# Kernel optimization log

Hardware: AMD Instinct MI355X
Metric: run time of the kernel (lower is better)

Reference implementation:

```python
import jax, jax.numpy as jnp
import numpy as np

B, T, I = 256, 1024, 64
P, E, NOUT = 256, 128, 64
K = 2
TEMP = 8.0
LN_EPS = 1e-5


def setup_inputs() -> dict:
    key = jax.random.key(0)
    ks = jax.random.split(key, 10)
    lim_in = 1.0 / np.sqrt(I)
    lim_e = 1.0 / np.sqrt(E)
    return {
        "x": jax.random.normal(ks[0], (B, T, I), dtype=jnp.float32),
        "pointer_init": jax.random.uniform(ks[1], (B,), dtype=jnp.float32) * P,
        "W_in": jax.random.uniform(ks[2], (E, I), minval=-lim_in, maxval=lim_in),
        "b_in": jax.random.uniform(ks[3], (E,), minval=-lim_in, maxval=lim_in),
        "ln_w": jnp.ones((E,), jnp.float32),
        "ln_b": jnp.zeros((E,), jnp.float32),
        "jump_dest": jax.random.uniform(ks[4], (P,), dtype=jnp.float32) * P,
        "Wg": jax.random.uniform(ks[5], (1, E), minval=-lim_e, maxval=lim_e),
        "bg": jax.random.uniform(ks[6], (1,), minval=-lim_e, maxval=lim_e),
        "context_strength": jnp.float32(0.2),
        "Wo": jax.random.uniform(ks[7], (NOUT, E), minval=-lim_e, maxval=lim_e),
        "bo": jax.random.uniform(ks[8], (NOUT,), minval=-lim_e, maxval=lim_e),
    }


def _layer_norm(h, w, b):
    mu = jnp.mean(h, axis=-1, keepdims=True)
    var = jnp.mean((h - mu) ** 2, axis=-1, keepdims=True)
    return (h - mu) * jax.lax.rsqrt(var + LN_EPS) * w + b


def reference(x, pointer_init, W_in, b_in, ln_w, ln_b, jump_dest, Wg, bg, context_strength, Wo, bo):
    Bsz = x.shape[0]
    nP = jump_dest.shape[0]
    offsets = jnp.arange(-K, K + 1, dtype=jnp.int32)  # [5]
    batch_idx = jnp.arange(Bsz)[:, None]               # [B,1]
    ctx_scale = jax.nn.sigmoid(context_strength)
    half = nP / 2.0

    def step(carry, x_t):
        mem, hid, ptr = carry                          # [B,P,E], [B,E], [B]
        emb = jnp.tanh(x_t @ W_in.T + b_in)            # [B,E]
        base = jnp.clip(jnp.floor(ptr).astype(jnp.int32), 0, nP - 1)
        idx = jnp.mod(base[:, None] + offsets[None, :], nP)  # [B,5]
        delta = jnp.mod(idx.astype(x_t.dtype) - ptr[:, None] + half, nP) - half
        w = jax.nn.softmax(-(delta ** 2) / TEMP, axis=1)     # [B,5]
        nbh = jnp.take_along_axis(mem, idx[:, :, None], axis=1)  # [B,5,E]
        ctx = jnp.sum(w[:, :, None] * nbh, axis=1)               # [B,E]
        su = jnp.tanh(emb + ctx_scale * ctx + hid)               # [B,E]
        hid_new = _layer_norm(su, ln_w, ln_b)
        mem_new = mem.at[batch_idx, idx].add(w[:, :, None] * su[:, None, :])
        cur = jnp.clip(ptr.astype(jnp.int32), 0, nP - 1)
        jt = jump_dest[cur]                                      # [B]
        jl = (su @ Wg.T + bg)[:, 0]                              # [B]
        probs = jax.nn.sigmoid(jl)
        sj = (probs > 0.5).astype(x_t.dtype) - jax.lax.stop_gradient(probs) + probs
        walk = jnp.mod(ptr + 1.0, nP)
        ptr_new = jnp.where(sj > 0.5, jt, walk)
        return (mem_new, hid_new, ptr_new), None

    mem0 = jnp.zeros((Bsz, nP, W_in.shape[0]), x.dtype)
    hid0 = jnp.zeros((Bsz, W_in.shape[0]), x.dtype)
    (mem, hid, ptr), _ = jax.lax.scan(step, (mem0, hid0, pointer_init), jnp.swapaxes(x, 0, 1))
    logits = hid @ Wo.T + bo
    return logits
```

## Files before the change

kernel.cpp:

```cpp
#include <hip/hip_runtime.h>
#include <math.h>

#define Bn    256
#define Tn    1024
#define In    64
#define Pn    256
#define En    128
#define NOUTn 64
#define LN_EPS 1e-5f

#define C1f 0.3606737602222409f
#define K1f 0.8824969025845955f
#define K2f 0.6065306597126334f

typedef float f32x2 __attribute__((ext_vector_type(2)));

__device__ __forceinline__ float tanh_fast(float x) {
    float e = __builtin_amdgcn_exp2f(x * 2.88539008177793f);
    return 1.0f - 2.0f * __builtin_amdgcn_rcpf(e + 1.0f);
}
__device__ __forceinline__ f32x2 tanh2(f32x2 x) {
    f32x2 e;
    e[0] = __builtin_amdgcn_exp2f(x[0] * 2.88539008177793f);
    e[1] = __builtin_amdgcn_exp2f(x[1] * 2.88539008177793f);
    f32x2 r;
    r[0] = __builtin_amdgcn_rcpf(e[0] + 1.0f);
    r[1] = __builtin_amdgcn_rcpf(e[1] + 1.0f);
    return 1.0f - 2.0f * r;
}

template<int CTRL, int RMASK>
__device__ __forceinline__ float dpp_add(float x) {
    return x + __int_as_float(__builtin_amdgcn_update_dpp(
        0, __float_as_int(x), CTRL, RMASK, 0xF, false));
}
__device__ __forceinline__ void wave_sum64_x3(float& x, float& y, float& z) {
#define LVL(C, R) x = dpp_add<C, R>(x); y = dpp_add<C, R>(y); z = dpp_add<C, R>(z);
    LVL(0x111, 0xF)
    LVL(0x112, 0xF)
    LVL(0x114, 0xF)
    LVL(0x118, 0xF)
    LVL(0x142, 0xA)
    LVL(0x143, 0xC)
#undef LVL
    x = __int_as_float(__builtin_amdgcn_readlane(__float_as_int(x), 63));
    y = __int_as_float(__builtin_amdgcn_readlane(__float_as_int(y), 63));
    z = __int_as_float(__builtin_amdgcn_readlane(__float_as_int(z), 63));
}

#define LDSF_FLOATS (Pn * En + Pn)
#define LDSF_BYTES  (LDSF_FLOATS * 4)

__global__ __launch_bounds__(192, 1)
void fused_kernel(const float* __restrict__ x,
                  const float* __restrict__ pointer_init,
                  const float* __restrict__ W_in, const float* __restrict__ b_in,
                  const float* __restrict__ ln_w, const float* __restrict__ ln_b,
                  const float* __restrict__ jump_dest,
                  const float* __restrict__ Wg,  const float* __restrict__ bg,
                  const float* __restrict__ cs_ptr,
                  const float* __restrict__ Wo,  const float* __restrict__ bo,
                  float* __restrict__ emb4, float* __restrict__ out) {
    extern __shared__ float lds[];
    float* mem = lds;
    float* jd  = lds + Pn * En;

    const int b   = blockIdx.x;
    const int tid = threadIdx.x;

    if (tid >= 64) {
        const int p     = tid - 64;
        const int t_oct = p >> 4;
        const int e0    = p & 15;
        float be[8];
        #pragma unroll
        for (int j = 0; j < 8; ++j) be[j] = b_in[e0 + 16 * j];

        const float* xb   = x + (size_t)b * Tn * In;
        float*       dstb = emb4 + ((size_t)b << 17);

#define PRODUCE(K) {                                                          \
    const int t0 = (K) * 64 + t_oct * 8;                                      \
    const float4* xr = (const float4*)(xb + t0 * In);      \
    float acc[8][8];                                                          \
    _Pragma("unroll")                                                         \
    for (int tt = 0; tt < 8; ++tt)                                            \
        _Pragma("unroll")                                                     \
        for (int j = 0; j < 8; ++j) acc[tt][j] = 0.f;                         \
    for (int i4 = 0; i4 < 16; ++i4) {                                         \
        float4 xv[8];                                                         \
        _Pragma("unroll")                                                     \
        for (int tt = 0; tt < 8; ++tt) xv[tt] = xr[tt * 16 + i4];             \
        float4 wf[8];                                                         \
        _Pragma("unroll")                                                     \
        for (int j = 0; j < 8; ++j)                                           \
            wf[j] = *(const float4*)(W_in + (e0 + 16 * j) * In + i4 * 4);     \
        _Pragma("unroll")                                                     \
        for (int tt = 0; tt < 8; ++tt)                                        \
            _Pragma("unroll")                                                 \
            for (int j = 0; j < 8; ++j) {                                     \
                acc[tt][j] += xv[tt].x * wf[j].x;                             \
                acc[tt][j] += xv[tt].y * wf[j].y;                             \
                acc[tt][j] += xv[tt].z * wf[j].z;                             \
                acc[tt][j] += xv[tt].w * wf[j].w;                             \
            }                                                                 \
    }                                                                         \
    const int tb0 = t0 >> 2;                                                  \
    _Pragma("unroll")                                                         \
    for (int j = 0; j < 8; ++j) {                                             \
        const int e = e0 + 16 * j;                                            \
        _Pragma("unroll")                                                     \
        for (int tb = 0; tb < 2; ++tb) {                                      \
            float4 o;                                                         \
            o.x = tanh_fast(acc[tb * 4 + 0][j] + be[j]);                      \
            o.y = tanh_fast(acc[tb * 4 + 1][j] + be[j]);                      \
            o.z = tanh_fast(acc[tb * 4 + 2][j] + be[j]);                      \
            o.w = tanh_fast(acc[tb * 4 + 3][j] + be[j]);                      \
            *(float4*)&dstb[((size_t)(tb0 + tb) * 128 + e) * 4] = o;          \
        }                                                                     \
    }                                                                         \
}
        PRODUCE(0)
        PRODUCE(1)
        __syncthreads();
        for (int k = 0; k < 16; ++k) {
            if (k + 2 < 16) PRODUCE(k + 2)
            __syncthreads();
        }
#undef PRODUCE
        __syncthreads();
        return;
    }

    const int l = tid;

    float4* m4 = (float4*)mem;
    for (int i = l; i < Pn * En / 4; i += 64) m4[i] = make_float4(0.f, 0.f, 0.f, 0.f);
    for (int i = l; i < Pn; i += 64) jd[i] = jump_dest[i];

    const f32x2 lnw = {ln_w[l], ln_w[l + 64]};
    const f32x2 lnb = {ln_b[l], ln_b[l + 64]};
    const f32x2 wg  = {Wg[l],   Wg[l + 64]};
    const float bgs = bg[0];
    const float cs  = 1.0f / (1.0f + expf(-cs_ptr[0]));
    f32x2 hid = {0.f, 0.f};

    float* myb = mem + 2 * l;

    float jl      = 1.0f;
    float jt_cur  = pointer_init[b];
    float ptrW    = 0.f;
    int   baseW   = 0;
    float jtW_pre = 0.f;
    float z0 = 0.f, z1 = 0.f, z2 = 1.f, z3 = 0.f, z4 = 0.f, inv = 1.f;
    f32x2 wnb0 = {0,0}, wnb1 = {0,0}, wnb2 = {0,0}, wnb3 = {0,0}, wnb4 = {0,0};
    float *wp0 = myb, *wp1 = myb, *wp2 = myb, *wp3 = myb, *wp4 = myb;

    __syncthreads();

    const float4* e40 = (const float4*)(emb4 + ((size_t)b << 17)) + l;
    const float4* e41 = e40 + 64;
    float4 A0 = e40[0],   A1 = e41[0];
    float4 B0 = e40[128], B1 = e41[128];

#define SSTEP(EC0, EC1) {                                                      \
    float ptr; int base;                                                       \
    f32x2 nb0, nb1, nb2, nb3, nb4;                                             \
    float *p0, *p1, *p2, *p3, *p4;                                             \
    float jt_nxt;                                                              \
    if (__builtin_amdgcn_readfirstlane(__float_as_int(jl)) > 0) {              \
                                     \
        ptr  = jt_cur;                                                         \
        base = (int)ptr; base = base > 255 ? 255 : base;                       \
        p0 = mem + (((base + 254) & 255) << 7) + 2 * l;                        \
        p1 = mem + (((base + 255) & 255) << 7) + 2 * l;                        \
        p2 = mem + (base << 7) + 2 * l;                                        \
        p3 = mem + (((base + 1) & 255) << 7) + 2 * l;                          \
        p4 = mem + (((base + 2) & 255) << 7) + 2 * l;                          \
        nb0 = *(f32x2*)p0; nb1 = *(f32x2*)p1; nb2 = *(f32x2*)p2;               \
        nb3 = *(f32x2*)p3; nb4 = *(f32x2*)p4;                                  \
        jt_nxt = jd[base];                                                     \
        const float frac = ptr - (float)base;                                  \
        const float r  = __builtin_amdgcn_exp2f(frac * C1f);                   \
        const float ri = __builtin_amdgcn_exp2f(-frac * C1f);                  \
        z0 = K2f * ri * ri; z1 = K1f * ri; z2 = 1.0f;                          \
        z3 = K1f * r;       z4 = K2f * r * r;                                  \
        inv = __builtin_amdgcn_rcpf(((z0 + z1) + (z2 + z3)) + z4);             \
    } else {                                                                   \
          \
        ptr = ptrW; base = baseW;                                              \
        nb0 = wnb0; nb1 = wnb1; nb2 = wnb2; nb3 = wnb3; nb4 = wnb4;            \
        p0 = wp0; p1 = wp1; p2 = wp2; p3 = wp3; p4 = wp4;                      \
        jt_nxt = jtW_pre;                                                      \
    }                                                                          \
    const f32x2 ctx = inv * (((nb0 * z0 + nb1 * z1) + (nb2 * z2 + nb3 * z3))   \
                             + nb4 * z4);                                      \
    f32x2 em; em[0] = (EC0); em[1] = (EC1);                                    \
    const f32x2 su = tanh2(em + cs * ctx + hid);                               \
    const f32x2 g  = su * inv;                                                 \
    const f32x2 m0v = nb0 + z0 * g, m1v = nb1 + z1 * g, m2v = nb2 + z2 * g,    \
                m3v = nb3 + z3 * g, m4v = nb4 + z4 * g;                        \
    *(f32x2*)p0 = m0v; *(f32x2*)p1 = m1v; *(f32x2*)p2 = m2v;                   \
    *(f32x2*)p3 = m3v; *(f32x2*)p4 = m4v;                                      \
     \
    baseW = (base + 1) & 255;                                                  \
    ptrW  = ptr + 1.0f; if (ptrW >= 256.0f) ptrW -= 256.0f;                    \
    wnb0 = m1v; wnb1 = m2v; wnb2 = m3v; wnb3 = m4v;                            \
    wp0 = p1; wp1 = p2; wp2 = p3; wp3 = p4;                                    \
    wp4 = mem + (((base + 3) & 255) << 7) + 2 * l;                             \
    wnb4 = *(f32x2*)wp4;                                                       \
    jtW_pre = jd[baseW];                                                       \
    jt_cur  = jt_nxt;                                                          \
                                                   \
    float s1 = su[0] + su[1];                                                  \
    const f32x2 sq = su * su;  float s2 = sq[0] + sq[1];                       \
    const f32x2 sg = su * wg;  float s3 = sg[0] + sg[1];                       \
    wave_sum64_x3(s1, s2, s3);                                                 \
    const float mu   = s1 * (1.0f / En);                                       \
    const float var  = s2 * (1.0f / En) - mu * mu;                             \
    const float rstd = __builtin_amdgcn_rsqf(var + LN_EPS);                    \
    hid = (su - mu) * rstd * lnw + lnb;                                        \
    jl  = s3 + bgs;                                                            \
}

    for (int k = 0; k < 16; ++k) {
        for (int tbi = 0; tbi < 16; ++tbi) {
            const int tb = k * 16 + tbi;
            const int tp = tb + 2 > 255 ? 255 : tb + 2;
            float4 C0 = e40[tp << 7];
            float4 C1 = e41[tp << 7];
            SSTEP(A0.x, A1.x)
            SSTEP(A0.y, A1.y)
            SSTEP(A0.z, A1.z)
            SSTEP(A0.w, A1.w)
            A0 = B0; A1 = B1; B0 = C0; B1 = C1;
        }
        __syncthreads();
    }
#undef SSTEP

    mem[l] = hid[0]; mem[64 + l] = hid[1];
    __syncthreads();
    const float4* w4 = (const float4*)(Wo + l * En);
    const float4* h4 = (const float4*)mem;
    float a0 = 0.f, a1 = 0.f, a2 = 0.f, a3 = 0.f;
    #pragma unroll
    for (int i = 0; i < En / 4; ++i) {
        float4 wv = w4[i]; float4 hv = h4[i];
        a0 += wv.x * hv.x; a1 += wv.y * hv.y; a2 += wv.z * hv.z; a3 += wv.w * hv.w;
    }
    out[b * NOUTn + l] = (a0 + a1) + (a2 + a3) + bo[l];
}

#define LDS_FLOATS (Pn*En + 2*En + 2*In + Pn)
#define LDS_BYTES  (LDS_FLOATS * 4)

__global__ __launch_bounds__(192, 1)
void ring_kernel(const float* __restrict__ x,
                 const float* __restrict__ pointer_init,
                 const float* __restrict__ W_in,
                 const float* __restrict__ b_in,
                 const float* __restrict__ ln_w,
                 const float* __restrict__ ln_b,
                 const float* __restrict__ jump_dest,
                 const float* __restrict__ Wg,
                 const float* __restrict__ bg,
                 const float* __restrict__ cs_ptr,
                 const float* __restrict__ Wo,
                 const float* __restrict__ bo,
                 float* __restrict__ out)
{
    extern __shared__ float lds[];
    float* mem  = lds;
    float* embb = mem + Pn * En;
    float* xb   = embb + 2 * En;
    float* jd   = xb + 2 * In;

    const int b   = blockIdx.x;
    const int tid = threadIdx.x;

    for (int i = tid; i < Pn * En; i += 192) mem[i] = 0.0f;
    for (int i = tid; i < Pn;      i += 192) jd[i]  = jump_dest[i];

    const float* xrow = x + (size_t)b * Tn * In;
    if (tid < 64) {
        xb[tid]      = xrow[tid];
        xb[In + tid] = xrow[In + tid];
    }
    __syncthreads();

    if (tid >= 64) {
        const int p = tid - 64;
        float wr[In];
        {
            const float4* w4 = (const float4*)(W_in + p * In);
            #pragma unroll
            for (int i = 0; i < In / 4; ++i) {
                float4 v = w4[i];
                wr[4*i+0] = v.x; wr[4*i+1] = v.y; wr[4*i+2] = v.z; wr[4*i+3] = v.w;
            }
        }
        const float bi = b_in[p];
        {
            float acc = bi;
            #pragma unroll
            for (int i = 0; i < In; ++i) acc += wr[i] * xb[i];
            embb[p] = tanhf(acc);
        }
        __syncthreads();
        for (int t = 0; t < Tn; ++t) {
            if (t + 1 < Tn) {
                const float* xc = xb + ((t + 1) & 1) * In;
                float acc = bi;
                #pragma unroll
                for (int i = 0; i < In; ++i) acc += wr[i] * xc[i];
                embb[((t + 1) & 1) * En + p] = tanhf(acc);
            }
            __syncthreads();
        }
    } else {
        const int l = tid;
        const float lnw0 = ln_w[l],      lnw1 = ln_w[l + 64];
        const float lnb0 = ln_b[l],      lnb1 = ln_b[l + 64];
        const float wg0  = Wg[l],        wg1  = Wg[l + 64];
        const float bgs  = bg[0];
        const float cs   = 1.0f / (1.0f + expf(-cs_ptr[0]));
        float hid0 = 0.0f, hid1 = 0.0f;
        float ptr  = pointer_init[b];
        __syncthreads();

        for (int t = 0; t < Tn; ++t) {
            const bool do_stage = (t + 2 < Tn);
            float xs = 0.0f;
            if (do_stage) xs = xrow[(t + 2) * In + l];

            const float* embc = embb + (t & 1) * En;

            int base = (int)floorf(ptr);
            base = base < 0 ? 0 : (base > Pn - 1 ? Pn - 1 : base);
            int cur = (int)ptr;
            cur = cur < 0 ? 0 : (cur > Pn - 1 ? Pn - 1 : cur);
            const float jt = jd[cur];

            const float frac = ptr - (float)base;
            int   idx[5];
            float wgt[5];
            float mx = -3.4e38f;
            #pragma unroll
            for (int j = 0; j < 5; ++j) {
                idx[j] = (base + j - 2 + Pn) & (Pn - 1);
                float d = (float)(j - 2) - frac;
                float s = -(d * d) * 0.125f;
                wgt[j] = s;
                mx = fmaxf(mx, s);
            }
            float se = 0.0f;
            #pragma unroll
            for (int j = 0; j < 5; ++j) { float ez = expf(wgt[j] - mx); wgt[j] = ez; se += ez; }
            const float inv = 1.0f / se;

            float nb0[5], nb1[5];
            #pragma unroll
            for (int j = 0; j < 5; ++j) {
                nb0[j] = mem[idx[j] * En + l];
                nb1[j] = mem[idx[j] * En + 64 + l];
            }
            float ctx0 = 0.0f, ctx1 = 0.0f;
            #pragma unroll
            for (int j = 0; j < 5; ++j) {
                const float w = wgt[j] * inv; wgt[j] = w;
                ctx0 += w * nb0[j];
                ctx1 += w * nb1[j];
            }

            const float su0 = tanhf(embc[l]      + cs * ctx0 + hid0);
            const float su1 = tanhf(embc[l + 64] + cs * ctx1 + hid1);

            #pragma unroll
            for (int j = 0; j < 5; ++j) {
                mem[idx[j] * En + l]      = nb0[j] + wgt[j] * su0;
                mem[idx[j] * En + 64 + l] = nb1[j] + wgt[j] * su1;
            }

            float s1 = su0 + su1;
            float s2 = su0 * su0 + su1 * su1;
            float s3 = su0 * wg0 + su1 * wg1;
            #pragma unroll
            for (int off = 32; off > 0; off >>= 1) {
                s1 += __shfl_xor(s1, off, 64);
                s2 += __shfl_xor(s2, off, 64);
                s3 += __shfl_xor(s3, off, 64);
            }

            const float mu   = s1 * (1.0f / En);
            const float var  = s2 * (1.0f / En) - mu * mu;
            const float rstd = rsqrtf(var + LN_EPS);
            hid0 = (su0 - mu) * rstd * lnw0 + lnb0;
            hid1 = (su1 - mu) * rstd * lnw1 + lnb1;

            const float jl = s3 + bgs;
            float walk = ptr + 1.0f;
            if (walk >= 256.0f) walk -= 256.0f;
            ptr = (jl > 0.0f) ? jt : walk;

            if (do_stage) xb[(t & 1) * In + l] = xs;
            __syncthreads();
        }
        embb[l]      = hid0;
        embb[l + 64] = hid1;
    }
    __syncthreads();

    if (tid < NOUTn) {
        const float* wrow = Wo + tid * En;
        float acc = bo[tid];
        #pragma unroll 4
        for (int e = 0; e < En; ++e) acc += embb[e] * wrow[e];
        out[b * NOUTn + tid] = acc;
    }
}

extern "C" void kernel_launch(void* const* d_in, const int* in_sizes, int n_in,
                              void* d_out, int out_size, void* d_ws, size_t ws_size,
                              hipStream_t stream) {
    const float* x            = (const float*)d_in[0];
    const float* pointer_init = (const float*)d_in[1];
    const float* W_in         = (const float*)d_in[2];
    const float* b_in         = (const float*)d_in[3];
    const float* ln_w         = (const float*)d_in[4];
    const float* ln_b         = (const float*)d_in[5];
    const float* jump_dest    = (const float*)d_in[6];
    const float* Wg           = (const float*)d_in[7];
    const float* bg           = (const float*)d_in[8];
    const float* cs           = (const float*)d_in[9];
    const float* Wo           = (const float*)d_in[10];
    const float* bo           = (const float*)d_in[11];
    float* out = (float*)d_out;

    const size_t emb_bytes = (size_t)Bn * Tn * En * sizeof(float);

    if (ws_size >= emb_bytes) {
        float* emb4 = (float*)d_ws;
        (void)hipFuncSetAttribute((const void*)fused_kernel,
                                  hipFuncAttributeMaxDynamicSharedMemorySize, LDSF_BYTES);
        fused_kernel<<<Bn, 192, LDSF_BYTES, stream>>>(
            x, pointer_init, W_in, b_in, ln_w, ln_b, jump_dest, Wg, bg, cs,
            Wo, bo, emb4, out);
    } else {
        (void)hipFuncSetAttribute((const void*)ring_kernel,
                                  hipFuncAttributeMaxDynamicSharedMemorySize, LDS_BYTES);
        ring_kernel<<<Bn, 192, LDS_BYTES, stream>>>(
            x, pointer_init, W_in, b_in, ln_w, ln_b, jump_dest, Wg, bg, cs, Wo, bo, out);
    }
}
```

Measured before the change: 504.6 us.

## Stage input embeddings in an LDS ring buffer instead of global workspace

```diff
diff --git a/kernel.cpp b/kernel.cpp
--- a/kernel.cpp
+++ b/kernel.cpp
@@ -48,83 +48,84 @@
     z = __int_as_float(__builtin_amdgcn_readlane(__float_as_int(z), 63));
 }
 
-#define LDSF_FLOATS (Pn * En + Pn)
-#define LDSF_BYTES  (LDSF_FLOATS * 4)
+#define STAGE_FLOATS (3 * 16 * En)
+#define LDSF_FLOATS  (Pn * En + Pn + STAGE_FLOATS)
+#define LDSF_BYTES   (LDSF_FLOATS * 4)
 
 __global__ __launch_bounds__(192, 1)
-void fused_kernel(const float* __restrict__ x,
-                  const float* __restrict__ pointer_init,
-                  const float* __restrict__ W_in, const float* __restrict__ b_in,
-                  const float* __restrict__ ln_w, const float* __restrict__ ln_b,
-                  const float* __restrict__ jump_dest,
-                  const float* __restrict__ Wg,  const float* __restrict__ bg,
-                  const float* __restrict__ cs_ptr,
-                  const float* __restrict__ Wo,  const float* __restrict__ bo,
-                  float* __restrict__ emb4, float* __restrict__ out) {
+void fused2_kernel(const float* __restrict__ x,
+                   const float* __restrict__ pointer_init,
+                   const float* __restrict__ W_in, const float* __restrict__ b_in,
+                   const float* __restrict__ ln_w, const float* __restrict__ ln_b,
+                   const float* __restrict__ jump_dest,
+                   const float* __restrict__ Wg,  const float* __restrict__ bg,
+                   const float* __restrict__ cs_ptr,
+                   const float* __restrict__ Wo,  const float* __restrict__ bo,
+                   float* __restrict__ out) {
     extern __shared__ float lds[];
     float* mem = lds;
     float* jd  = lds + Pn * En;
+    float* stg = lds + Pn * En + Pn;
 
     const int b   = blockIdx.x;
     const int tid = threadIdx.x;
 
     if (tid >= 64) {
-        const int p     = tid - 64;
-        const int t_oct = p >> 4;
-        const int e0    = p & 15;
-        float be[8];
+        const int p    = tid - 64;
+        const int tq   = p >> 5;
+        const int eidx = p & 31;
+        float be[4];
         #pragma unroll
-        for (int j = 0; j < 8; ++j) be[j] = b_in[e0 + 16 * j];
-
-        const float* xb   = x + (size_t)b * Tn * In;
-        float*       dstb = emb4 + ((size_t)b << 17);
-
-#define PRODUCE(K) {                                                          \
-    const int t0 = (K) * 64 + t_oct * 8;                                      \
+        for (int j = 0; j < 4; ++j) be[j] = b_in[eidx + 32 * j];
+        const float* xb = x + (size_t)b * Tn * In;
+
+#define PRODUCE(K, BUF) {                                                     \
+    const int t0 = (K) * 16 + tq * 4;                                         \
     const float4* xr = (const float4*)(xb + t0 * In);      \
-    float acc[8][8];                                                          \
+    float acc[4][4];                                                          \
     _Pragma("unroll")                                                         \
-    for (int tt = 0; tt < 8; ++tt)                                            \
-        _Pragma("unroll")                                                     \
-        for (int j = 0; j < 8; ++j) acc[tt][j] = 0.f;                         \
+    for (int tt = 0; tt < 4; ++tt)                                            \
+        _Pragma("unroll")                                                     \
+        for (int j = 0; j < 4; ++j) acc[tt][j] = 0.f;                         \
+    _Pragma("unroll")                                                         \
     for (int i4 = 0; i4 < 16; ++i4) {                                         \
-        float4 xv[8];                                                         \
-        _Pragma("unroll")                                                     \
-        for (int tt = 0; tt < 8; ++tt) xv[tt] = xr[tt * 16 + i4];             \
-        float4 wf[8];                                                         \
-        _Pragma("unroll")                                                     \
-        for (int j = 0; j < 8; ++j)                                           \
-            wf[j] = *(const float4*)(W_in + (e0 + 16 * j) * In + i4 * 4);     \
-        _Pragma("unroll")                                                     \
-        for (int tt = 0; tt < 8; ++tt)                                        \
+        float4 xv[4];                                                         \
+        _Pragma("unroll")                                                     \
+        for (int tt = 0; tt < 4; ++tt) xv[tt] = xr[tt * 16 + i4];             \
+        float4 wf[4];                                                         \
+        _Pragma("unroll")                                                     \
+        for (int j = 0; j < 4; ++j)                                           \
+            wf[j] = *(const float4*)(W_in + (eidx + 32 * j) * In + i4 * 4);   \
+        _Pragma("unroll")                                                     \
+        for (int tt = 0; tt < 4; ++tt)                                        \
             _Pragma("unroll")                                                 \
-            for (int j = 0; j < 8; ++j) {                                     \
+            for (int j = 0; j < 4; ++j) {                                     \
                 acc[tt][j] += xv[tt].x * wf[j].x;                             \
                 acc[tt][j] += xv[tt].y * wf[j].y;                             \
                 acc[tt][j] += xv[tt].z * wf[j].z;                             \
                 acc[tt][j] += xv[tt].w * wf[j].w;                             \
             }                                                                 \
     }                                                                         \
-    const int tb0 = t0 >> 2;                                                  \
+    float* sg = stg + (BUF) * 2048 + tq * 512;                                \
     _Pragma("unroll")                                                         \
-    for (int j = 0; j < 8; ++j) {                                             \
-        const int e = e0 + 16 * j;                                            \
-        _Pragma("unroll")                                                     \
-        for (int tb = 0; tb < 2; ++tb) {                                      \
-            float4 o;                                                         \
-            o.x = tanh_fast(acc[tb * 4 + 0][j] + be[j]);                      \
-            o.y = tanh_fast(acc[tb * 4 + 1][j] + be[j]);                      \
-            o.z = tanh_fast(acc[tb * 4 + 2][j] + be[j]);                      \
-            o.w = tanh_fast(acc[tb * 4 + 3][j] + be[j]);                      \
-            *(float4*)&dstb[((size_t)(tb0 + tb) * 128 + e) * 4] = o;          \
-        }                                                                     \
+    for (int j = 0; j < 4; ++j) {                                             \
+        float4 o;                                                             \
+        o.x = tanh_fast(acc[0][j] + be[j]);                                   \
+        o.y = tanh_fast(acc[1][j] + be[j]);                                   \
+        o.z = tanh_fast(acc[2][j] + be[j]);                                   \
+        o.w = tanh_fast(acc[3][j] + be[j]);                                   \
+        *(float4*)(sg + (eidx + 32 * j) * 4) = o;                             \
     }                                                                         \
 }
-        PRODUCE(0)
-        PRODUCE(1)
+        PRODUCE(0, 0)
+        PRODUCE(1, 1)
         __syncthreads();
-        for (int k = 0; k < 16; ++k) {
-            if (k + 2 < 16) PRODUCE(k + 2)
+        int buf = 2;
+        for (int k = 0; k < 64; ++k) {
+            if (k + 2 < 64) {
+                PRODUCE(k + 2, buf)
+                buf = (buf == 2) ? 0 : buf + 1;
+            }
             __syncthreads();
         }
 #undef PRODUCE
@@ -158,10 +159,9 @@
 
     __syncthreads();
 
-    const float4* e40 = (const float4*)(emb4 + ((size_t)b << 17)) + l;
-    const float4* e41 = e40 + 64;
-    float4 A0 = e40[0],   A1 = e41[0];
-    float4 B0 = e40[128], B1 = e41[128];
+    const float* sa0 = stg + 4 * l;
+    float4 A0 = *(const float4*)sa0;
+    float4 A1 = *(const float4*)(sa0 + 256);
 
 #define SSTEP(EC0, EC1) {                                                      \
     float ptr; int base;                                                       \
@@ -223,17 +223,19 @@
     jl  = s3 + bgs;                                                            \
 }
 
-    for (int k = 0; k < 16; ++k) {
-        for (int tbi = 0; tbi < 16; ++tbi) {
-            const int tb = k * 16 + tbi;
-            const int tp = tb + 2 > 255 ? 255 : tb + 2;
-            float4 C0 = e40[tp << 7];
-            float4 C1 = e41[tp << 7];
+    for (int k = 0; k < 64; ++k) {
+        #pragma unroll
+        for (int g = 0; g < 4; ++g) {
+            const int tb  = k * 4 + g;
+            int tbn = tb + 1; if (tbn > 255) tbn = 255;
+            const float* sb = stg + ((tbn >> 2) % 3) * 2048 + (tbn & 3) * 512 + 4 * l;
+            float4 B0 = *(const float4*)sb;
+            float4 B1 = *(const float4*)(sb + 256);
             SSTEP(A0.x, A1.x)
             SSTEP(A0.y, A1.y)
             SSTEP(A0.z, A1.z)
             SSTEP(A0.w, A1.w)
-            A0 = B0; A1 = B1; B0 = C0; B1 = C1;
+            A0 = B0; A1 = B1;
         }
         __syncthreads();
     }
@@ -250,174 +252,6 @@
         a0 += wv.x * hv.x; a1 += wv.y * hv.y; a2 += wv.z * hv.z; a3 += wv.w * hv.w;
     }
     out[b * NOUTn + l] = (a0 + a1) + (a2 + a3) + bo[l];
-}
-
-#define LDS_FLOATS (Pn*En + 2*En + 2*In + Pn)
-#define LDS_BYTES  (LDS_FLOATS * 4)
-
-__global__ __launch_bounds__(192, 1)
-void ring_kernel(const float* __restrict__ x,
-                 const float* __restrict__ pointer_init,
-                 const float* __restrict__ W_in,
-                 const float* __restrict__ b_in,
-                 const float* __restrict__ ln_w,
-                 const float* __restrict__ ln_b,
-                 const float* __restrict__ jump_dest,
-                 const float* __restrict__ Wg,
-                 const float* __restrict__ bg,
-                 const float* __restrict__ cs_ptr,
-                 const float* __restrict__ Wo,
-                 const float* __restrict__ bo,
-                 float* __restrict__ out)
-{
-    extern __shared__ float lds[];
-    float* mem  = lds;
-    float* embb = mem + Pn * En;
-    float* xb   = embb + 2 * En;
-    float* jd   = xb + 2 * In;
-
-    const int b   = blockIdx.x;
-    const int tid = threadIdx.x;
-
-    for (int i = tid; i < Pn * En; i += 192) mem[i] = 0.0f;
-    for (int i = tid; i < Pn;      i += 192) jd[i]  = jump_dest[i];
-
-    const float* xrow = x + (size_t)b * Tn * In;
-    if (tid < 64) {
-        xb[tid]      = xrow[tid];
-        xb[In + tid] = xrow[In + tid];
-    }
-    __syncthreads();
-
-    if (tid >= 64) {
-        const int p = tid - 64;
-        float wr[In];
-        {
-            const float4* w4 = (const float4*)(W_in + p * In);
-            #pragma unroll
-            for (int i = 0; i < In / 4; ++i) {
-                float4 v = w4[i];
-                wr[4*i+0] = v.x; wr[4*i+1] = v.y; wr[4*i+2] = v.z; wr[4*i+3] = v.w;
-            }
-        }
-        const float bi = b_in[p];
-        {
-            float acc = bi;
-            #pragma unroll
-            for (int i = 0; i < In; ++i) acc += wr[i] * xb[i];
-            embb[p] = tanhf(acc);
-        }
-        __syncthreads();
-        for (int t = 0; t < Tn; ++t) {
-            if (t + 1 < Tn) {
-                const float* xc = xb + ((t + 1) & 1) * In;
-                float acc = bi;
-                #pragma unroll
-                for (int i = 0; i < In; ++i) acc += wr[i] * xc[i];
-                embb[((t + 1) & 1) * En + p] = tanhf(acc);
-            }
-            __syncthreads();
-        }
-    } else {
-        const int l = tid;
-        const float lnw0 = ln_w[l],      lnw1 = ln_w[l + 64];
-        const float lnb0 = ln_b[l],      lnb1 = ln_b[l + 64];
-        const float wg0  = Wg[l],        wg1  = Wg[l + 64];
-        const float bgs  = bg[0];
-        const float cs   = 1.0f / (1.0f + expf(-cs_ptr[0]));
-        float hid0 = 0.0f, hid1 = 0.0f;
-        float ptr  = pointer_init[b];
-        __syncthreads();
-
-        for (int t = 0; t < Tn; ++t) {
-            const bool do_stage = (t + 2 < Tn);
-            float xs = 0.0f;
-            if (do_stage) xs = xrow[(t + 2) * In + l];
-
-            const float* embc = embb + (t & 1) * En;
-
-            int base = (int)floorf(ptr);
-            base = base < 0 ? 0 : (base > Pn - 1 ? Pn - 1 : base);
-            int cur = (int)ptr;
-            cur = cur < 0 ? 0 : (cur > Pn - 1 ? Pn - 1 : cur);
-            const float jt = jd[cur];
-
-            const float frac = ptr - (float)base;
-            int   idx[5];
-            float wgt[5];
-            float mx = -3.4e38f;
-            #pragma unroll
-            for (int j = 0; j < 5; ++j) {
-                idx[j] = (base + j - 2 + Pn) & (Pn - 1);
-                float d = (float)(j - 2) - frac;
-                float s = -(d * d) * 0.125f;
-                wgt[j] = s;
-                mx = fmaxf(mx, s);
-            }
-            float se = 0.0f;
-            #pragma unroll
-            for (int j = 0; j < 5; ++j) { float ez = expf(wgt[j] - mx); wgt[j] = ez; se += ez; }
-            const float inv = 1.0f / se;
-
-            float nb0[5], nb1[5];
-            #pragma unroll
-            for (int j = 0; j < 5; ++j) {
-                nb0[j] = mem[idx[j] * En + l];
-                nb1[j] = mem[idx[j] * En + 64 + l];
-            }
-            float ctx0 = 0.0f, ctx1 = 0.0f;
-            #pragma unroll
-            for (int j = 0; j < 5; ++j) {
-                const float w = wgt[j] * inv; wgt[j] = w;
-                ctx0 += w * nb0[j];
-                ctx1 += w * nb1[j];
-            }
-
-            const float su0 = tanhf(embc[l]      + cs * ctx0 + hid0);
-            const float su1 = tanhf(embc[l + 64] + cs * ctx1 + hid1);
-
-            #pragma unroll
-            for (int j = 0; j < 5; ++j) {
-                mem[idx[j] * En + l]      = nb0[j] + wgt[j] * su0;
-                mem[idx[j] * En + 64 + l] = nb1[j] + wgt[j] * su1;
-            }
-
-            float s1 = su0 + su1;
-            float s2 = su0 * su0 + su1 * su1;
-            float s3 = su0 * wg0 + su1 * wg1;
-            #pragma unroll
-            for (int off = 32; off > 0; off >>= 1) {
-                s1 += __shfl_xor(s1, off, 64);
-                s2 += __shfl_xor(s2, off, 64);
-                s3 += __shfl_xor(s3, off, 64);
-            }
-
-            const float mu   = s1 * (1.0f / En);
-            const float var  = s2 * (1.0f / En) - mu * mu;
-            const float rstd = rsqrtf(var + LN_EPS);
-            hid0 = (su0 - mu) * rstd * lnw0 + lnb0;
-            hid1 = (su1 - mu) * rstd * lnw1 + lnb1;
-
-            const float jl = s3 + bgs;
-            float walk = ptr + 1.0f;
-            if (walk >= 256.0f) walk -= 256.0f;
-            ptr = (jl > 0.0f) ? jt : walk;
-
-            if (do_stage) xb[(t & 1) * In + l] = xs;
-            __syncthreads();
-        }
-        embb[l]      = hid0;
-        embb[l + 64] = hid1;
-    }
-    __syncthreads();
-
-    if (tid < NOUTn) {
-        const float* wrow = Wo + tid * En;
-        float acc = bo[tid];
-        #pragma unroll 4
-        for (int e = 0; e < En; ++e) acc += embb[e] * wrow[e];
-        out[b * NOUTn + tid] = acc;
-    }
 }
 
 extern "C" void kernel_launch(void* const* d_in, const int* in_sizes, int n_in,
@@ -436,20 +270,11 @@
     const float* Wo           = (const float*)d_in[10];
     const float* bo           = (const float*)d_in[11];
     float* out = (float*)d_out;
-
-    const size_t emb_bytes = (size_t)Bn * Tn * En * sizeof(float);
-
-    if (ws_size >= emb_bytes) {
-        float* emb4 = (float*)d_ws;
-        (void)hipFuncSetAttribute((const void*)fused_kernel,
-                                  hipFuncAttributeMaxDynamicSharedMemorySize, LDSF_BYTES);
-        fused_kernel<<<Bn, 192, LDSF_BYTES, stream>>>(
-            x, pointer_init, W_in, b_in, ln_w, ln_b, jump_dest, Wg, bg, cs,
-            Wo, bo, emb4, out);
-    } else {
-        (void)hipFuncSetAttribute((const void*)ring_kernel,
-                                  hipFuncAttributeMaxDynamicSharedMemorySize, LDS_BYTES);
-        ring_kernel<<<Bn, 192, LDS_BYTES, stream>>>(
-            x, pointer_init, W_in, b_in, ln_w, ln_b, jump_dest, Wg, bg, cs, Wo, bo, out);
-    }
-}
+    (void)d_ws; (void)ws_size;
+
+    (void)hipFuncSetAttribute((const void*)fused2_kernel,
+                              hipFuncAttributeMaxDynamicSharedMemorySize, LDSF_BYTES);
+    fused2_kernel<<<Bn, 192, LDSF_BYTES, stream>>>(
+        x, pointer_init, W_in, b_in, ln_w, ln_b, jump_dest, Wg, bg, cs,
+        Wo, bo, out);
+}
```

New measurement: 472.2 us, median of 2. 6.4% less time.
